# Kernel tuning notes

Hardware: AMD Instinct MI355X
Metric: run time of the kernel (lower is better)

Reference implementation:

```python
import jax, jax.numpy as jnp
import numpy as np

SEQ, BATCH, D_MODEL, HEADS = 2048, 4, 1024, 16
D_K = D_MODEL // HEADS
SCALE = 1.0 / np.sqrt(D_K).astype(np.float32)


def setup_inputs() -> dict:
    key = jax.random.key(0)
    ks = jax.random.split(key, 12)
    s = 0.02
    inp = {
        "query": jax.random.normal(ks[0], (SEQ, BATCH, D_MODEL), jnp.float32),
        "key": jax.random.normal(ks[1], (SEQ, BATCH, D_MODEL), jnp.float32),
        "value": jax.random.normal(ks[2], (SEQ, BATCH, D_MODEL), jnp.float32),
        # causal mask [seq_q, seq_k, 1]; batch dim broadcasts per prepare_mask
        "mask": jnp.tril(jnp.ones((SEQ, SEQ), jnp.int32))[:, :, None],
        "Wq": jax.random.normal(ks[3], (D_MODEL, D_MODEL), jnp.float32) * s,
        "bq": jnp.zeros((D_MODEL,), jnp.float32),
        "Wk": jax.random.normal(ks[4], (D_MODEL, D_MODEL), jnp.float32) * s,
        "bk": jnp.zeros((D_MODEL,), jnp.float32),
        "Wv": jax.random.normal(ks[5], (D_MODEL, D_MODEL), jnp.float32) * s,
        "bv": jnp.zeros((D_MODEL,), jnp.float32),
        "Wo": jax.random.normal(ks[6], (D_MODEL, D_MODEL), jnp.float32) * s,
        "bo": jnp.zeros((D_MODEL,), jnp.float32),
    }
    return inp


def _heads(x, W, b):
    # [s, b, d_model] -> [s, b, h, d_k]
    y = jnp.einsum('sbd,de->sbe', x, W.T) + b
    return y.reshape(x.shape[0], x.shape[1], HEADS, D_K)


def reference(query, key, value, mask, Wq, bq, Wk, bk, Wv, bv, Wo, bo):
    seq_len, batch_size, _ = query.shape
    q = _heads(query, Wq, bq)
    k = _heads(key, Wk, bk)
    v = _heads(value, Wv, bv)
    # scores [i, j, b, h]
    scores = jnp.einsum('ibhd,jbhd->ijbh', q, k) * SCALE
    m = mask[:, :, :, None]  # [sq, sk, b_or_1, 1]
    scores = jnp.where(m == 0, jnp.float32(-jnp.inf), scores)
    attn = jax.nn.softmax(scores, axis=1)  # softmax over key dim j
    x = jnp.einsum('ijbh,jbhd->ibhd', attn, v)
    x = x.reshape(seq_len, batch_size, D_MODEL)
    return jnp.einsum('sbd,de->sbe', x, Wo.T) + bo
```

## Files before the change

### kernel.cpp

```cpp
#include <hip/hip_runtime.h>
#include <hip/hip_bf16.h>

#define SEQ 2048
#define BATCH 4
#define DM 1024
#define HEADS 16
#define DK 64
#define NBH 64
#define SC_LOG2E (0.125f * 1.4426950408889634f)

typedef unsigned short u16;
typedef __attribute__((ext_vector_type(8))) short bf16x8;
typedef __attribute__((ext_vector_type(4))) float f32x4;

__device__ inline u16 f2bf(float f) {
    unsigned int u = __builtin_bit_cast(unsigned int, f);
    u += 0x7fffu + ((u >> 16) & 1u);
    return (u16)(u >> 16);
}
__device__ inline float fexp2(float x) {
    float r; asm("v_exp_f32 %0, %1" : "=v"(r) : "v"(x)); return r;
}
__device__ inline unsigned pkbf(float a, float b) {
    unsigned r; asm("v_cvt_pk_bf16_f32 %0, %1, %2" : "=v"(r) : "v"(a), "v"(b)); return r;
}

__global__ __launch_bounds__(256)
void conv_w(const float* __restrict__ wq, const float* __restrict__ wk,
            const float* __restrict__ wv, const float* __restrict__ wo,
            u16* __restrict__ ow)
{
    const size_t W8 = (size_t)DM * DM / 8;
    size_t i = (size_t)blockIdx.x * 256 + threadIdx.x;
    int wsel = (int)(i >> 17);
    size_t off = i & (W8 - 1);
    const float* src = wsel == 0 ? wq : wsel == 1 ? wk : wsel == 2 ? wv : wo;
    u16* dst = ow + (size_t)wsel * DM * DM;
    float4 a = ((const float4*)src)[off * 2];
    float4 b = ((const float4*)src)[off * 2 + 1];
    uint4 w;
    w.x = pkbf(a.x, a.y); w.y = pkbf(a.z, a.w);
    w.z = pkbf(b.x, b.y); w.w = pkbf(b.z, b.w);
    *(uint4*)(dst + off * 8) = w;
}

__device__ inline void gstage(const u16* __restrict__ src, u16* dst,
                              int wave, int lane) {
    #pragma unroll
    for (int i = 0; i < 4; ++i) {
        int ci = (i * 4 + wave) * 64 + lane;
        int row = ci >> 3, ch = ci & 7;
        const u16* g = src + (size_t)row * 1024 + ((ch ^ (row & 7)) << 3);
        u16* l = dst + (i * 4 + wave) * 512;
        __builtin_amdgcn_global_load_lds(
            (const __attribute__((address_space(1))) unsigned int*)g,
            (__attribute__((address_space(3))) unsigned int*)l, 16, 0, 0);
    }
}
__device__ inline bf16x8 rdt(const u16* t, int row, int ch) {
    return *(const bf16x8*)(t + row * 64 + ((ch ^ (row & 7)) << 3));
}

__global__ __launch_bounds__(256, 2)
void gemm_bf(const u16* __restrict__ A, const u16* __restrict__ B,
             const float* __restrict__ bias, float* __restrict__ Out)
{
    __shared__ __align__(16) u16 sA[2][128 * 64];
    __shared__ __align__(16) u16 sB[2][128 * 64];
    const int tid  = threadIdx.x;
    const int lane = tid & 63, wave = tid >> 6;
    const int wr = (wave >> 1) * 64, wc = (wave & 1) * 64;
    const int l15 = lane & 15, lg = lane >> 4;
    const int row0 = blockIdx.x * 128, col0 = blockIdx.y * 128;
    const u16* Abase = A + (size_t)row0 * 1024;
    const u16* Bbase = B + (size_t)col0 * 1024;

    f32x4 acc[4][4];
    #pragma unroll
    for (int m = 0; m < 4; ++m)
        #pragma unroll
        for (int n = 0; n < 4; ++n) acc[m][n] = (f32x4){0.f, 0.f, 0.f, 0.f};

    gstage(Abase, sA[0], wave, lane);
    gstage(Bbase, sB[0], wave, lane);
    __syncthreads();

    int cur = 0;
    for (int kt = 0; kt < 16; ++kt) {
        if (kt < 15) {
            gstage(Abase + (kt + 1) * 64, sA[cur ^ 1], wave, lane);
            gstage(Bbase + (kt + 1) * 64, sB[cur ^ 1], wave, lane);
        }
        #pragma unroll
        for (int s = 0; s < 2; ++s) {
            bf16x8 af[4], bf[4];
            #pragma unroll
            for (int m = 0; m < 4; ++m)
                af[m] = rdt(sA[cur], wr + m * 16 + l15, s * 4 + lg);
            #pragma unroll
            for (int n = 0; n < 4; ++n)
                bf[n] = rdt(sB[cur], wc + n * 16 + l15, s * 4 + lg);
            __builtin_amdgcn_s_setprio(1);
            #pragma unroll
            for (int m = 0; m < 4; ++m)
                #pragma unroll
                for (int n = 0; n < 4; ++n)
                    acc[m][n] = __builtin_amdgcn_mfma_f32_16x16x32_bf16(
                        af[m], bf[n], acc[m][n], 0, 0, 0);
            __builtin_amdgcn_s_setprio(0);
        }
        __syncthreads();
        cur ^= 1;
    }
    #pragma unroll
    for (int m = 0; m < 4; ++m)
        #pragma unroll
        for (int n = 0; n < 4; ++n)
            #pragma unroll
            for (int r = 0; r < 4; ++r) {
                int R = row0 + wr + m * 16 + lg * 4 + r;
                int E = col0 + wc + n * 16 + l15;
                Out[(size_t)R * 1024 + E] = acc[m][n][r] + bias[E];
            }
}

__global__ __launch_bounds__(256, 3)
void gemm_qkv(const float* __restrict__ q, const float* __restrict__ k,
              const float* __restrict__ v, const u16* __restrict__ Wbf,
              const float* __restrict__ bq, const float* __restrict__ bk,
              const float* __restrict__ bv,
              u16* __restrict__ Qb, u16* __restrict__ Kb, u16* __restrict__ Vt)
{
    __shared__ __align__(16) u16 sA[128 * 64];
    __shared__ __align__(16) u16 sB[2][128 * 64];
    const int g = blockIdx.y >> 3;
    const float* A    = g == 0 ? q  : g == 1 ? k  : v;
    const float* bias = g == 0 ? bq : g == 1 ? bk : bv;
    u16* Out          = g == 0 ? Qb : g == 1 ? Kb : Vt;
    const u16* B = Wbf + (size_t)g * DM * DM;
    const float oscale = g == 0 ? SC_LOG2E : 1.0f;
    const bool vmode = (g == 2);

    const int tid  = threadIdx.x;
    const int lane = tid & 63, wave = tid >> 6;
    const int wr = (wave >> 1) * 64, wc = (wave & 1) * 64;
    const int l15 = lane & 15, lg = lane >> 4;
    const int row0 = blockIdx.x * 128, col0 = (blockIdx.y & 7) * 128;
    const int arow = tid >> 4;
    const int ach  = tid & 15;
    const float* Ag = A + (size_t)(row0 + arow) * 1024 + ach * 4;
    const u16* Bbase = B + (size_t)col0 * 1024;

    f32x4 acc[4][4];
    #pragma unroll
    for (int m = 0; m < 4; ++m)
        #pragma unroll
        for (int n = 0; n < 4; ++n) acc[m][n] = (f32x4){0.f, 0.f, 0.f, 0.f};

    auto loadA = [&](int kt, float4* r) {
        #pragma unroll
        for (int i = 0; i < 8; ++i)
            r[i] = *(const float4*)(Ag + (size_t)i * 16 * 1024 + kt * 64);
    };
    auto writeA = [&](const float4* r) {
        const int c16 = ach >> 1, half = ach & 1;
        #pragma unroll
        for (int i = 0; i < 8; ++i) {
            int row = arow + 16 * i;
            uint2 w;
            w.x = pkbf(r[i].x, r[i].y);
            w.y = pkbf(r[i].z, r[i].w);
            *(uint2*)(sA + row * 64 + ((c16 ^ (row & 7)) << 3) + half * 4) = w;
        }
    };

    {
        float4 a0[8];
        loadA(0, a0);
        gstage(Bbase, sB[0], wave, lane);
        writeA(a0);
    }
    __syncthreads();

    int cur = 0;
    for (int kt = 0; kt < 16; ++kt) {
        float4 an[8];
        const bool pre = (kt < 15);
        if (pre) {
            loadA(kt + 1, an);
            gstage(Bbase + (kt + 1) * 64, sB[cur ^ 1], wave, lane);
        }
        #pragma unroll
        for (int s = 0; s < 2; ++s) {
            bf16x8 af[4], bf[4];
            #pragma unroll
            for (int m = 0; m < 4; ++m)
                af[m] = rdt(sA, wr + m * 16 + l15, s * 4 + lg);
            #pragma unroll
            for (int n = 0; n < 4; ++n)
                bf[n] = rdt(sB[cur], wc + n * 16 + l15, s * 4 + lg);
            __builtin_amdgcn_s_setprio(1);
            #pragma unroll
            for (int m = 0; m < 4; ++m)
                #pragma unroll
                for (int n = 0; n < 4; ++n)
                    acc[m][n] = __builtin_amdgcn_mfma_f32_16x16x32_bf16(
                        af[m], bf[n], acc[m][n], 0, 0, 0);
            __builtin_amdgcn_s_setprio(0);
        }
        __syncthreads();
        if (pre) writeA(an);
        __syncthreads();
        cur ^= 1;
    }

    #pragma unroll
    for (int m = 0; m < 4; ++m)
        #pragma unroll
        for (int n = 0; n < 4; ++n)
            #pragma unroll
            for (int r = 0; r < 4; ++r) {
                int R = row0 + wr + m * 16 + lg * 4 + r;
                int E = col0 + wc + n * 16 + l15;
                float val = (acc[m][n][r] + bias[E]) * oscale;
                int s = R >> 2, b = R & 3, hh = E >> 6, d = E & 63;
                size_t idx = vmode
                    ? ((size_t)(b * HEADS + hh) * DK + d) * SEQ + s
                    : ((size_t)(b * HEADS + hh) * SEQ + s) * DK + d;
                Out[idx] = f2bf(val);
            }
}

__device__ inline void stage_tile(const u16* __restrict__ srcRow0, int srcStride,
                                  u16* tile, int wave, int lane) {
    #pragma unroll
    for (int i = 0; i < 2; ++i) {
        int row = wave * 16 + i * 8 + (lane >> 3);
        int chunk = (lane & 7) ^ (row & 7);
        const u16* g = srcRow0 + (size_t)row * srcStride + chunk * 8;
        u16* l = tile + (wave * 16 + i * 8) * 64;
        __builtin_amdgcn_global_load_lds(
            (const __attribute__((address_space(1))) unsigned int*)g,
            (__attribute__((address_space(3))) unsigned int*)l, 16, 0, 0);
    }
}
__device__ inline bf16x8 tread(const u16* tile, int row, int chunk) {
    return *(const bf16x8*)((const char*)tile + row * 128 + ((chunk ^ (row & 7)) << 4));
}

__global__ __launch_bounds__(256, 4)
void attn_fwd(const u16* __restrict__ Q, const u16* __restrict__ K,
              const u16* __restrict__ V, u16* __restrict__ X)
{
    __shared__ __align__(16) u16 sK[2][4096];
    __shared__ __align__(16) u16 sV[2][4096];
    __shared__ __align__(16) u16 plds[4][16 * 64];

    const int lin = blockIdx.x + 16 * blockIdx.y;
    const int xcd = lin & 7, ii = lin >> 3;
    const int bh  = (ii & 7) | (xcd << 3);
    const int tA  = ii >> 3;
    const int tB  = 31 - tA;
    const int b = bh >> 4, h = bh & 15;
    const int lane = threadIdx.x & 63, wave = threadIdx.x >> 6;
    const int l15 = lane & 15, lg = lane >> 4;
    const int qloc = wave * 16 + l15;
    const int swz = (l15 & 7) << 4;
    const u16* Qh = Q + (size_t)bh * SEQ * DK;
    const u16* Kh = K + (size_t)bh * SEQ * DK;
    const u16* Vh = V + (size_t)bh * SEQ * DK;

    const int qA = tA * 64 + wave * 16, qB = tB * 64 + wave * 16;
    const bf16x8 qfA0 = *(const bf16x8*)&Qh[(size_t)(qA + l15) * DK + lg * 8];
    const bf16x8 qfA1 = *(const bf16x8*)&Qh[(size_t)(qA + l15) * DK + 32 + lg * 8];
    const bf16x8 qfB0 = *(const bf16x8*)&Qh[(size_t)(qB + l15) * DK + lg * 8];
    const bf16x8 qfB1 = *(const bf16x8*)&Qh[(size_t)(qB + l15) * DK + 32 + lg * 8];

    f32x4 oA[4], oB[4];
    #pragma unroll
    for (int n = 0; n < 4; ++n) {
        oA[n] = (f32x4){0.f, 0.f, 0.f, 0.f};
        oB[n] = (f32x4){0.f, 0.f, 0.f, 0.f};
    }
    float lsA = 0.f, lsB = 0.f;
    u16* pw = &plds[wave][0];

    auto compute = [&](const u16* kt, const u16* vt,
                       const bf16x8& q0v, const bf16x8& q1v,
                       f32x4* o, float& ls, bool diag) {
        f32x4 sc[4];
        #pragma unroll
        for (int c = 0; c < 4; ++c) sc[c] = (f32x4){0.f, 0.f, 0.f, 0.f};

        __builtin_amdgcn_s_setprio(1);
        #pragma unroll
        for (int c = 0; c < 4; ++c) {
            bf16x8 k0 = tread(kt, 16 * c + l15, lg);
            bf16x8 k1 = tread(kt, 16 * c + l15, 4 + lg);
            sc[c] = __builtin_amdgcn_mfma_f32_16x16x32_bf16(k0, q0v, sc[c], 0, 0, 0);
            sc[c] = __builtin_amdgcn_mfma_f32_16x16x32_bf16(k1, q1v, sc[c], 0, 0, 0);
        }
        __builtin_amdgcn_s_setprio(0);

        #pragma unroll
        for (int c = 0; c < 4; ++c) {
            float p[4];
            #pragma unroll
            for (int r = 0; r < 4; ++r) {
                float e = fexp2(sc[c][r]);
                if (diag) {
                    int kl = 16 * c + 4 * lg + r;
                    e = (kl <= qloc) ? e : 0.f;
                }
                p[r] = e;
                ls += e;
            }
            uint2 w;
            w.x = pkbf(p[0], p[1]);
            w.y = pkbf(p[2], p[3]);
            *(uint2*)((char*)pw + l15 * 128 + ((32 * c + 8 * lg) ^ swz)) = w;
        }
        asm volatile("s_waitcnt lgkmcnt(0)" ::: "memory");
        __builtin_amdgcn_sched_barrier(0);
        bf16x8 pf0 = *(const bf16x8*)((const char*)pw + l15 * 128 + ((16 * lg) ^ swz));
        bf16x8 pf1 = *(const bf16x8*)((const char*)pw + l15 * 128 + ((64 + 16 * lg) ^ swz));

        __builtin_amdgcn_s_setprio(1);
        #pragma unroll
        for (int n = 0; n < 4; ++n) {
            bf16x8 v0 = tread(vt, 16 * n + l15, lg);
            bf16x8 v1 = tread(vt, 16 * n + l15, 4 + lg);
            o[n] = __builtin_amdgcn_mfma_f32_16x16x32_bf16(pf0, v0, o[n], 0, 0, 0);
            o[n] = __builtin_amdgcn_mfma_f32_16x16x32_bf16(pf1, v1, o[n], 0, 0, 0);
        }
        __builtin_amdgcn_s_setprio(0);
    };

    stage_tile(Kh, DK, sK[0], wave, lane);
    stage_tile(Vh, SEQ, sV[0], wave, lane);
    __syncthreads();

    const int nst = tB + 1;
    int cur = 0;
    for (int blk = 0; blk < nst; ++blk) {
        if (blk + 1 < nst) {
            stage_tile(Kh + (size_t)(blk + 1) * 64 * DK, DK, sK[cur ^ 1], wave, lane);
            stage_tile(Vh + (blk + 1) * 64, SEQ, sV[cur ^ 1], wave, lane);
        }
        if (blk <= tA)
            compute(sK[cur], sV[cur], qfA0, qfA1, oA, lsA, blk == tA);
        compute(sK[cur], sV[cur], qfB0, qfB1, oB, lsB, blk == tB);
        __syncthreads();
        cur ^= 1;
    }

    auto finish = [&](f32x4* o, float ls, int q0) {
        float tot = ls;
        tot += __shfl_xor(tot, 16, 64);
        tot += __shfl_xor(tot, 32, 64);
        float inv[4];
        #pragma unroll
        for (int r = 0; r < 4; ++r)
            inv[r] = 1.0f / __shfl(tot, lg * 4 + r, 64);
        #pragma unroll
        for (int n = 0; n < 4; ++n)
            #pragma unroll
            for (int r = 0; r < 4; ++r) {
                const int i = q0 + lg * 4 + r;
                X[((size_t)i * BATCH + b) * DM + h * DK + 16 * n + l15] =
                    f2bf(o[n][r] * inv[r]);
            }
    };
    finish(oA, lsA, qA);
    finish(oB, lsB, qB);
}

extern "C" void kernel_launch(void* const* d_in, const int* in_sizes, int n_in,
                              void* d_out, int out_size, void* d_ws, size_t ws_size,
                              hipStream_t stream) {
    const float* query = (const float*)d_in[0];
    const float* key   = (const float*)d_in[1];
    const float* value = (const float*)d_in[2];
    const float* Wq = (const float*)d_in[4];
    const float* bq = (const float*)d_in[5];
    const float* Wk = (const float*)d_in[6];
    const float* bk = (const float*)d_in[7];
    const float* Wv = (const float*)d_in[8];
    const float* bv = (const float*)d_in[9];
    const float* Wo = (const float*)d_in[10];
    const float* bo = (const float*)d_in[11];

    const size_t NELEM = (size_t)SEQ * BATCH * DM;
    const size_t WM    = (size_t)DM * DM;
    u16* Qb  = (u16*)d_ws;
    u16* Kb  = Qb + NELEM;
    u16* Vt  = Kb + NELEM;
    u16* Xb  = Vt + NELEM;
    u16* Wbf = Xb + NELEM;

    dim3 gb(256);
    hipLaunchKernelGGL(conv_w, dim3(2048), gb, 0, stream, Wq, Wk, Wv, Wo, Wbf);
    hipLaunchKernelGGL(gemm_qkv, dim3(64, 24), gb, 0, stream,
                       query, key, value, Wbf, bq, bk, bv, Qb, Kb, Vt);
    hipLaunchKernelGGL(attn_fwd, dim3(16, NBH), gb, 0, stream, Qb, Kb, Vt, Xb);
    hipLaunchKernelGGL(gemm_bf, dim3(64, 8), gb, 0, stream,
                       Xb, Wbf + 3 * WM, bo, (float*)d_out);
}
```

Before: 163.5 us.

## Stage GEMM A tile through registers to cut LDS and raise occupancy

Result: slower. 167.0 us (+2.2%).

```diff
diff --git a/kernel.cpp b/kernel.cpp
--- a/kernel.cpp
+++ b/kernel.cpp
@@ -61,18 +61,20 @@
     return *(const bf16x8*)(t + row * 64 + ((ch ^ (row & 7)) << 3));
 }
 
-__global__ __launch_bounds__(256, 2)
+__global__ __launch_bounds__(256, 3)
 void gemm_bf(const u16* __restrict__ A, const u16* __restrict__ B,
              const float* __restrict__ bias, float* __restrict__ Out)
 {
-    __shared__ __align__(16) u16 sA[2][128 * 64];
+    __shared__ __align__(16) u16 sA[128 * 64];
     __shared__ __align__(16) u16 sB[2][128 * 64];
     const int tid  = threadIdx.x;
     const int lane = tid & 63, wave = tid >> 6;
     const int wr = (wave >> 1) * 64, wc = (wave & 1) * 64;
     const int l15 = lane & 15, lg = lane >> 4;
     const int row0 = blockIdx.x * 128, col0 = blockIdx.y * 128;
-    const u16* Abase = A + (size_t)row0 * 1024;
+    const int arow = tid >> 3;
+    const int ach  = tid & 7;
+    const u16* Ag = A + (size_t)(row0 + arow) * 1024 + ach * 8;
     const u16* Bbase = B + (size_t)col0 * 1024;
 
     f32x4 acc[4][4];
@@ -81,14 +83,33 @@
         #pragma unroll
         for (int n = 0; n < 4; ++n) acc[m][n] = (f32x4){0.f, 0.f, 0.f, 0.f};
 
-    gstage(Abase, sA[0], wave, lane);
-    gstage(Bbase, sB[0], wave, lane);
+    auto loadA = [&](int kt, bf16x8* r) {
+        #pragma unroll
+        for (int i = 0; i < 4; ++i)
+            r[i] = *(const bf16x8*)(Ag + (size_t)i * 32 * 1024 + kt * 64);
+    };
+    auto writeA = [&](const bf16x8* r) {
+        #pragma unroll
+        for (int i = 0; i < 4; ++i) {
+            int row = arow + 32 * i;
+            *(bf16x8*)(sA + row * 64 + ((ach ^ (row & 7)) << 3)) = r[i];
+        }
+    };
+
+    {
+        bf16x8 a0[4];
+        loadA(0, a0);
+        gstage(Bbase, sB[0], wave, lane);
+        writeA(a0);
+    }
     __syncthreads();
 
     int cur = 0;
     for (int kt = 0; kt < 16; ++kt) {
-        if (kt < 15) {
-            gstage(Abase + (kt + 1) * 64, sA[cur ^ 1], wave, lane);
+        bf16x8 an[4];
+        const bool pre = (kt < 15);
+        if (pre) {
+            loadA(kt + 1, an);
             gstage(Bbase + (kt + 1) * 64, sB[cur ^ 1], wave, lane);
         }
         #pragma unroll
@@ -96,7 +117,7 @@
             bf16x8 af[4], bf[4];
             #pragma unroll
             for (int m = 0; m < 4; ++m)
-                af[m] = rdt(sA[cur], wr + m * 16 + l15, s * 4 + lg);
+                af[m] = rdt(sA, wr + m * 16 + l15, s * 4 + lg);
             #pragma unroll
             for (int n = 0; n < 4; ++n)
                 bf[n] = rdt(sB[cur], wc + n * 16 + l15, s * 4 + lg);
@@ -109,6 +130,8 @@
                         af[m], bf[n], acc[m][n], 0, 0, 0);
             __builtin_amdgcn_s_setprio(0);
         }
+        __syncthreads();
+        if (pre) writeA(an);
         __syncthreads();
         cur ^= 1;
     }
```

## Deepen QKV projection GEMM pipeline with two-stage A register prefetch and explicit waitcnts

Applied to the files above, without the earlier changes.

New measurement: 320.7 us. +96.2%, slower.

```diff
diff --git a/kernel.cpp b/kernel.cpp
--- a/kernel.cpp
+++ b/kernel.cpp
@@ -173,23 +173,7 @@
             *(uint2*)(sA + row * 64 + ((c16 ^ (row & 7)) << 3) + half * 4) = w;
         }
     };
-
-    {
-        float4 a0[8];
-        loadA(0, a0);
-        gstage(Bbase, sB[0], wave, lane);
-        writeA(a0);
-    }
-    __syncthreads();
-
-    int cur = 0;
-    for (int kt = 0; kt < 16; ++kt) {
-        float4 an[8];
-        const bool pre = (kt < 15);
-        if (pre) {
-            loadA(kt + 1, an);
-            gstage(Bbase + (kt + 1) * 64, sB[cur ^ 1], wave, lane);
-        }
+    auto mfma_step = [&](const u16* sBc) {
         #pragma unroll
         for (int s = 0; s < 2; ++s) {
             bf16x8 af[4], bf[4];
@@ -198,7 +182,7 @@
                 af[m] = rdt(sA, wr + m * 16 + l15, s * 4 + lg);
             #pragma unroll
             for (int n = 0; n < 4; ++n)
-                bf[n] = rdt(sB[cur], wc + n * 16 + l15, s * 4 + lg);
+                bf[n] = rdt(sBc, wc + n * 16 + l15, s * 4 + lg);
             __builtin_amdgcn_s_setprio(1);
             #pragma unroll
             for (int m = 0; m < 4; ++m)
@@ -208,11 +192,50 @@
                         af[m], bf[n], acc[m][n], 0, 0, 0);
             __builtin_amdgcn_s_setprio(0);
         }
-        __syncthreads();
-        if (pre) writeA(an);
-        __syncthreads();
+    };
+
+    float4 aP[8], aN[8];
+    {
+        float4 a0[8];
+        loadA(0, a0);
+        gstage(Bbase, sB[0], wave, lane);
+        asm volatile("s_waitcnt vmcnt(0)" ::: "memory");
+        __builtin_amdgcn_sched_barrier(0);
+        writeA(a0);
+        loadA(1, aP);
+        asm volatile("s_waitcnt lgkmcnt(0)" ::: "memory");
+        __builtin_amdgcn_sched_barrier(0);
+        __builtin_amdgcn_s_barrier();
+    }
+
+    int cur = 0;
+    #pragma unroll 2
+    for (int kt = 0; kt < 14; ++kt) {
+        gstage(Bbase + (kt + 1) * 64, sB[cur ^ 1], wave, lane);
+        loadA(kt + 2, aN);
+        mfma_step(sB[cur]);
+        asm volatile("s_waitcnt vmcnt(8)" ::: "memory");
+        __builtin_amdgcn_sched_barrier(0);
+        __builtin_amdgcn_s_barrier();
+        writeA(aP);
+        #pragma unroll
+        for (int j = 0; j < 8; ++j) aP[j] = aN[j];
+        asm volatile("s_waitcnt lgkmcnt(0)" ::: "memory");
+        __builtin_amdgcn_sched_barrier(0);
+        __builtin_amdgcn_s_barrier();
         cur ^= 1;
     }
+    gstage(Bbase + 15 * 64, sB[cur ^ 1], wave, lane);
+    mfma_step(sB[cur]);
+    asm volatile("s_waitcnt vmcnt(0)" ::: "memory");
+    __builtin_amdgcn_sched_barrier(0);
+    __builtin_amdgcn_s_barrier();
+    writeA(aP);
+    asm volatile("s_waitcnt lgkmcnt(0)" ::: "memory");
+    __builtin_amdgcn_sched_barrier(0);
+    __builtin_amdgcn_s_barrier();
+    cur ^= 1;
+    mfma_step(sB[cur]);
 
     #pragma unroll
     for (int m = 0; m < 4; ++m)
```
